# Kernel optimization log

Measured on AMD Instinct MI355X. Metric: run time of the kernel, lower is better.

Reference implementation:

```python
import jax, jax.numpy as jnp
import numpy as np

N_NODES = 100000
N_EDGES = 3200000
IN_DIM = 11
HID = 32


def setup_inputs() -> dict:
    key = jax.random.key(0)
    ks = jax.random.split(key, 12)
    inp = {
        "x": jax.random.normal(ks[0], (N_NODES, IN_DIM), dtype=jnp.float32),
        "edge_index": jax.random.randint(ks[1], (2, N_EDGES), 0, N_NODES, dtype=jnp.int32),
        "batch": jnp.zeros((N_NODES,), dtype=jnp.int32),
        # GCNConv layer 1 (11 -> 32)
        "W1": jax.random.normal(ks[2], (IN_DIM, HID), dtype=jnp.float32) / np.sqrt(IN_DIM),
        "b1": jnp.zeros((HID,), dtype=jnp.float32),
        # GCNConv layer 2 (32 -> 32)
        "W2": jax.random.normal(ks[3], (HID, HID), dtype=jnp.float32) / np.sqrt(HID),
        "b2": jnp.zeros((HID,), dtype=jnp.float32),
        # output MLP: 32 -> 16 -> 1
        "Wo1": jax.random.normal(ks[4], (HID, HID // 2), dtype=jnp.float32) / np.sqrt(HID),
        "bo1": jnp.zeros((HID // 2,), dtype=jnp.float32),
        "Wo2": jax.random.normal(ks[5], (HID // 2, 1), dtype=jnp.float32) / np.sqrt(HID // 2),
        "bo2": jnp.zeros((1,), dtype=jnp.float32),
    }
    return inp


def _gcn_norm(edge_index, n_nodes):
    # Add self-loops and compute symmetric normalization (PyG GCNConv default).
    loops = jnp.arange(n_nodes, dtype=edge_index.dtype)
    src = jnp.concatenate([edge_index[0], loops])
    dst = jnp.concatenate([edge_index[1], loops])
    ones = jnp.ones_like(dst, dtype=jnp.float32)
    deg = jax.ops.segment_sum(ones, dst, num_segments=n_nodes)  # degree of A+I on target side
    dinv = jax.lax.rsqrt(deg)  # deg >= 1 thanks to self-loops
    norm = dinv[src] * dinv[dst]  # [E+N]
    return src, dst, norm


def _gcn_conv(x, W, b, src, dst, norm, n_nodes):
    xw = x @ W                                   # transform first (small dim)
    msg = norm[:, None] * xw[src]                # gather + scale  [E+N, H]
    agg = jax.ops.segment_sum(msg, dst, num_segments=n_nodes)  # scatter-add
    return agg + b


def reference(x, edge_index, batch, W1, b1, W2, b2, Wo1, bo1, Wo2, bo2):
    n = x.shape[0]
    src, dst, norm = _gcn_norm(edge_index, n)
    h = jax.nn.relu(_gcn_conv(x, W1, b1, src, dst, norm, n))
    # F.dropout(training=self.training) is identity in eval mode
    h = jax.nn.relu(_gcn_conv(h, W2, b2, src, dst, norm, n))
    h = jax.nn.elu(h @ Wo1 + bo1)
    out = h @ Wo2 + bo2
    return out.squeeze(-1)  # [N]
```

## Files before the change

kernel.cpp:

```cpp
#include <hip/hip_runtime.h>
#include <hip/hip_fp16.h>
#include <math.h>

#define N_NODES 100000
#define N_EDGES 3200000
#define IN_DIM 11
#define HID 32
#define HID2 16
#define SCHUNK 100352
#define BINSHIFT 8
#define BINSZ 256
#define NB 391
#define CHUNK 6144
#define NCH 521
#define NCH1 522
#define FCAP 9216

__device__ __forceinline__ int wincl(int v) {
    int lane = threadIdx.x & 63;
#pragma unroll
    for (int d = 1; d < 64; d <<= 1) {
        int u = __shfl_up(v, d, 64);
        v += (lane >= d) ? u : 0;
    }
    return v;
}

__device__ __forceinline__ int blkexcl512(int v, int* wtot) {
    int t = threadIdx.x, lane = t & 63, w = t >> 6;
    int inc = wincl(v);
    if (lane == 63) wtot[w] = inc;
    __syncthreads();
    if (t < 8) {
        int x = wtot[t], ix = x;
#pragma unroll
        for (int d = 1; d < 8; d <<= 1) {
            int u = __shfl_up(ix, d, 64);
            ix += (lane >= d) ? u : 0;
        }
        wtot[t] = ix - x;
    }
    __syncthreads();
    return inc - v + wtot[w];
}

__global__ __launch_bounds__(256) void k_hist(const int* __restrict__ ei,
                                              int* __restrict__ cnthist) {
    __shared__ int h[NB];
    int t = threadIdx.x;
    for (int i = t; i < NB; i += 256) h[i] = 0;
    __syncthreads();
    int b0 = blockIdx.x * CHUNK;
    int n = N_EDGES - b0; if (n > CHUNK) n = CHUNK;
    for (int e = t * 4; e < n; e += 1024) {
        int4 d4 = *(const int4*)(ei + N_EDGES + b0 + e);
        atomicAdd(&h[d4.x >> BINSHIFT], 1);
        atomicAdd(&h[d4.y >> BINSHIFT], 1);
        atomicAdd(&h[d4.z >> BINSHIFT], 1);
        atomicAdd(&h[d4.w >> BINSHIFT], 1);
    }
    __syncthreads();
    for (int i = t; i < NB; i += 256)
        cnthist[i * NCH1 + blockIdx.x] = h[i];
}

__global__ __launch_bounds__(256) void k_colscan(int* __restrict__ cnthist,
                                                 int* __restrict__ colsum) {
    __shared__ int wtot[4];
    int i = blockIdx.x;
    int t = threadIdx.x;
    int lane = t & 63;
    int v[4];
    int s4 = 0;
#pragma unroll
    for (int u = 0; u < 4; ++u) {
        int idx = t * 4 + u;
        v[u] = (idx < NCH) ? cnthist[i * NCH1 + idx] : 0;
        s4 += v[u];
    }
    int inc = wincl(s4);
    if (lane == 63) wtot[t >> 6] = inc;
    __syncthreads();
    if (t < 4) {
        int x = wtot[t], ix = x;
#pragma unroll
        for (int d = 1; d < 4; d <<= 1) {
            int u2 = __shfl_up(ix, d, 64);
            ix += (lane >= d) ? u2 : 0;
        }
        wtot[t] = ix - x;
    }
    __syncthreads();
    int base = inc - s4 + wtot[t >> 6];
#pragma unroll
    for (int u = 0; u < 4; ++u) {
        int idx = t * 4 + u;
        if (idx < NCH) cnthist[i * NCH1 + idx] = base;
        base += v[u];
    }
    if (t == 255) {
        cnthist[i * NCH1 + NCH] = base;
        colsum[i] = base;
    }
}

__global__ __launch_bounds__(512) void k_scanbins(const int* __restrict__ colsum,
                                                  int* __restrict__ binbase) {
    __shared__ int wtot[8];
    int t = threadIdx.x;
    int v = (t < NB) ? colsum[t] : 0;
    int pre = blkexcl512(v, wtot);
    if (t < NB) binbase[t] = pre;
    if (t == 0) binbase[NB] = N_EDGES;
}

__global__ __launch_bounds__(512) void k_binscatter(const int* __restrict__ ei,
                                                    const int* __restrict__ binbase,
                                                    const int* __restrict__ cnthist,
                                                    unsigned* __restrict__ binbuf) {
    __shared__ unsigned       srecS[CHUNK];
    __shared__ unsigned short sbinS[CHUNK];
    __shared__ int h[NB], rl[NB], gb[NB];
    __shared__ int wtot[8];
    int t = threadIdx.x;
    int b0 = blockIdx.x * CHUNK;
    int n = N_EDGES - b0; if (n > CHUNK) n = CHUNK;
    int pre_b = 0, c = 0;
    if (t < NB) {
        pre_b = cnthist[t * NCH1 + blockIdx.x];
        c = cnthist[t * NCH1 + blockIdx.x + 1] - pre_b;
    }
    int rlv = blkexcl512(c, wtot);
    if (t < NB) {
        rl[t] = rlv;
        gb[t] = binbase[t] + pre_b;
        h[t] = 0;
    }
    __syncthreads();
    for (int e = t; e < n; e += 512) {
        int d = ei[N_EDGES + b0 + e];
        int s = ei[b0 + e];
        int b = d >> BINSHIFT;
        int p = rl[b] + atomicAdd(&h[b], 1);
        srecS[p] = (unsigned)s | ((unsigned)(d & (BINSZ - 1)) << 17);
        sbinS[p] = (unsigned short)b;
    }
    __syncthreads();
    for (int p = t; p < n; p += 512) {
        int b = sbinS[p];
        binbuf[gb[b] + (p - rl[b])] = srecS[p];
    }
}

__global__ __launch_bounds__(512) void k_binfill(const unsigned* __restrict__ binbuf,
                                                 const int* __restrict__ binbase,
                                                 int* __restrict__ rowstart,
                                                 float* __restrict__ dinv,
                                                 int* __restrict__ csr_src) {
    int bb = blockIdx.x;
    int b = bb >> 1;
    int half = bb & 1;
    int t = threadIdx.x;
    __shared__ unsigned srec[FCAP];
    __shared__ int cnt[BINSZ], rloc[BINSZ], cur[BINSZ], wtot[8];
    int ebeg = binbase[b], eend = binbase[b + 1];
    int m = eend - ebeg;
    if (t < BINSZ) cnt[t] = 0;
    __syncthreads();
    for (int e = t; e < m; e += 512) {
        unsigned v = binbuf[ebeg + e];
        if (e < FCAP) srec[e] = v;
        atomicAdd(&cnt[v >> 17], 1);
    }
    __syncthreads();
    int c = (t < BINSZ) ? cnt[t] : 0;
    int pre = blkexcl512(c, wtot);
    if (t < BINSZ) {
        rloc[t] = pre;
        cur[t] = 0;
        int node = b * BINSZ + t;
        if ((t >> 7) == half && node < N_NODES) {
            rowstart[node] = ebeg + pre;
            dinv[node] = rsqrtf((float)c + 1.0f);
        }
    }
    if (bb == 0 && t == 0) rowstart[N_NODES] = N_EDGES;
    __syncthreads();
    for (int e = t; e < m; e += 512) {
        unsigned vv = (e < FCAP) ? srec[e] : binbuf[ebeg + e];
        int dl = vv >> 17;
        if ((dl >> 7) == half) {
            int p = ebeg + rloc[dl] + atomicAdd(&cur[dl], 1);
            csr_src[p] = (int)(vv & 0x1FFFFu);
        }
    }
}

__global__ void k_xw1(const float* __restrict__ x, const float* __restrict__ W1,
                      const float* __restrict__ dinv, __half* __restrict__ xwh) {
    int t = blockIdx.x * blockDim.x + threadIdx.x;
    int node = t >> 5;
    int j = t & 31;
    __shared__ float sW[IN_DIM * HID];
    __shared__ float sx[8 * IN_DIM];
    for (int i = threadIdx.x; i < IN_DIM * HID; i += 256) sW[i] = W1[i];
    int base = blockIdx.x * 8;
    if (threadIdx.x < 8 * IN_DIM) sx[threadIdx.x] = x[base * IN_DIM + threadIdx.x];
    __syncthreads();
    int ln = node - base;
    float acc = 0.0f;
#pragma unroll
    for (int k = 0; k < IN_DIM; ++k)
        acc += sx[ln * IN_DIM + k] * sW[k * HID + j];
    xwh[t] = __float2half(dinv[node] * acc);
}

__device__ __forceinline__ void accum8(float* __restrict__ acc, const uint4 v) {
    float2 f0 = __half22float2(*(const __half2*)&v.x);
    float2 f1 = __half22float2(*(const __half2*)&v.y);
    float2 f2 = __half22float2(*(const __half2*)&v.z);
    float2 f3 = __half22float2(*(const __half2*)&v.w);
    acc[0] += f0.x; acc[1] += f0.y;
    acc[2] += f1.x; acc[3] += f1.y;
    acc[4] += f2.x; acc[5] += f2.y;
    acc[6] += f3.x; acc[7] += f3.y;
}

__device__ __forceinline__ void edge_accum8(int beg, int end, int q, int oj,
                                            const int* __restrict__ csr_src,
                                            const __half* __restrict__ xwh,
                                            float* __restrict__ acc) {
#pragma unroll
    for (int k = 0; k < 8; ++k) acc[k] = 0.0f;
    int e = beg;
    for (; e + 32 <= end; e += 32) {
        int s0 = csr_src[e + q];
        int s1 = csr_src[e + 8 + q];
        int s2 = csr_src[e + 16 + q];
        int s3 = csr_src[e + 24 + q];
        uint4 v0 = *(const uint4*)(xwh + ((s0 << 5) | oj));
        uint4 v1 = *(const uint4*)(xwh + ((s1 << 5) | oj));
        uint4 v2 = *(const uint4*)(xwh + ((s2 << 5) | oj));
        uint4 v3 = *(const uint4*)(xwh + ((s3 << 5) | oj));
        accum8(acc, v0); accum8(acc, v1); accum8(acc, v2); accum8(acc, v3);
    }
    if (e + 16 <= end) {
        int s0 = csr_src[e + q];
        int s1 = csr_src[e + 8 + q];
        uint4 v0 = *(const uint4*)(xwh + ((s0 << 5) | oj));
        uint4 v1 = *(const uint4*)(xwh + ((s1 << 5) | oj));
        accum8(acc, v0); accum8(acc, v1);
        e += 16;
    }
    if (e + 8 <= end) {
        int s0 = csr_src[e + q];
        uint4 v0 = *(const uint4*)(xwh + ((s0 << 5) | oj));
        accum8(acc, v0);
        e += 8;
    }
    if (e + q < end) {
        int s0 = csr_src[e + q];
        uint4 v0 = *(const uint4*)(xwh + ((s0 << 5) | oj));
        accum8(acc, v0);
    }
#pragma unroll
    for (int m = 4; m <= 16; m <<= 1) {
#pragma unroll
        for (int k = 0; k < 8; ++k) acc[k] += __shfl_xor(acc[k], m);
    }
}

__global__ __launch_bounds__(256) void k_gather_xw2(const int* __restrict__ rowstart,
                                                    const float* __restrict__ dinv,
                                                    const int* __restrict__ csr_src,
                                                    const __half* __restrict__ xwh1,
                                                    const float* __restrict__ b1,
                                                    const float* __restrict__ W2,
                                                    __half* __restrict__ xwh2) {
    __shared__ float sW2[HID * HID];
    __shared__ float sA[8][33];
    __shared__ float sH[8][33];
    for (int i = threadIdx.x; i < HID * HID; i += 256) sW2[i] = W2[i];

    int ln = threadIdx.x >> 5;
    int node = blockIdx.x * 8 + ln;
    int l = threadIdx.x & 31;
    int q = l >> 2;
    int oj = (l & 3) << 3;

    float acc[8];
    edge_accum8(rowstart[node], rowstart[node + 1], q, oj, csr_src, xwh1, acc);
    if (q == 0) {
#pragma unroll
        for (int k = 0; k < 8; ++k) sA[ln][oj + k] = acc[k];
    }
    __syncthreads();

    int j = l;
    float dd = dinv[node];
    float hv = dd * (sA[ln][j] + __half2float(xwh1[node * HID + j])) + b1[j];
    sH[ln][j] = hv > 0.0f ? hv : 0.0f;
    __syncthreads();

    float a2 = 0.0f;
#pragma unroll
    for (int k = 0; k < HID; ++k) a2 += sH[ln][k] * sW2[k * HID + j];
    xwh2[node * HID + j] = __float2half(dd * a2);
}

__global__ __launch_bounds__(256) void k_gather_mlp(const int* __restrict__ rowstart,
                                                    const float* __restrict__ dinv,
                                                    const int* __restrict__ csr_src,
                                                    const __half* __restrict__ xwh,
                                                    const float* __restrict__ b2,
                                                    const float* __restrict__ Wo1,
                                                    const float* __restrict__ bo1,
                                                    const float* __restrict__ Wo2,
                                                    const float* __restrict__ bo2,
                                                    float* __restrict__ out) {
    __shared__ float sW1[HID * HID2];
    __shared__ float sb1[HID2];
    __shared__ float sW2v[HID2];
    __shared__ float sb2[HID];
    __shared__ float sA[8][33];
    __shared__ float sH[8][33];
    for (int i = threadIdx.x; i < HID * HID2; i += 256) sW1[i] = Wo1[i];
    if (threadIdx.x < HID2) {
        sb1[threadIdx.x] = bo1[threadIdx.x];
        sW2v[threadIdx.x] = Wo2[threadIdx.x];
    }
    if (threadIdx.x < HID) sb2[threadIdx.x] = b2[threadIdx.x];

    int ln = threadIdx.x >> 5;
    int node = blockIdx.x * 8 + ln;
    int l = threadIdx.x & 31;
    int q = l >> 2;
    int oj = (l & 3) << 3;

    float acc[8];
    edge_accum8(rowstart[node], rowstart[node + 1], q, oj, csr_src, xwh, acc);
    if (q == 0) {
#pragma unroll
        for (int k = 0; k < 8; ++k) sA[ln][oj + k] = acc[k];
    }
    __syncthreads();

    int j = l;
    float dd = dinv[node];
    float hv = dd * (sA[ln][j] + __half2float(xwh[node * HID + j])) + sb2[j];
    sH[ln][j] = hv > 0.0f ? hv : 0.0f;
    __syncthreads();

    float val = 0.0f;
    if (j < HID2) {
        float a = sb1[j];
#pragma unroll
        for (int k = 0; k < HID; ++k) a += sH[ln][k] * sW1[k * HID2 + j];
        a = a > 0.0f ? a : (expf(a) - 1.0f);
        val = a * sW2v[j];
    }
#pragma unroll
    for (int d = 16; d >= 1; d >>= 1) val += __shfl_down(val, d, 32);
    if (j == 0) out[node] = val + bo2[0];
}

extern "C" void kernel_launch(void* const* d_in, const int* in_sizes, int n_in,
                              void* d_out, int out_size, void* d_ws, size_t ws_size,
                              hipStream_t stream) {
    const float* x   = (const float*)d_in[0];
    const int*   ei  = (const int*)d_in[1];
    const float* W1  = (const float*)d_in[3];
    const float* b1  = (const float*)d_in[4];
    const float* W2  = (const float*)d_in[5];
    const float* b2  = (const float*)d_in[6];
    const float* Wo1 = (const float*)d_in[7];
    const float* bo1 = (const float*)d_in[8];
    const float* Wo2 = (const float*)d_in[9];
    const float* bo2 = (const float*)d_in[10];
    float* out = (float*)d_out;

    int*      colsum   = (int*)d_ws;
    int*      binbase  = colsum + 512;
    int*      rowstart = binbase + 512;
    float*    dinv     = (float*)(rowstart + SCHUNK);
    int*      csr_src  = (int*)(dinv + SCHUNK);
    unsigned* binbuf   = (unsigned*)(csr_src + N_EDGES);
    __half*   XWH1     = (__half*)(binbuf + N_EDGES);
    __half*   XWH2     = XWH1 + (size_t)N_NODES * HID;
    int*      cnthist  = csr_src;

    const int BT = 256;
    int gNH  = (N_NODES * HID + BT - 1) / BT;
    int gG   = N_NODES / 8;

    k_hist      <<<NCH, BT, 0, stream>>>(ei, cnthist);
    k_colscan   <<<NB, BT, 0, stream>>>(cnthist, colsum);
    k_scanbins  <<<1, 512, 0, stream>>>(colsum, binbase);
    k_binscatter<<<NCH, 512, 0, stream>>>(ei, binbase, cnthist, binbuf);
    k_binfill   <<<2 * NB, 512, 0, stream>>>(binbuf, binbase, rowstart, dinv, csr_src);

    k_xw1<<<gNH, BT, 0, stream>>>(x, W1, dinv, XWH1);
    k_gather_xw2<<<gG, BT, 0, stream>>>(rowstart, dinv, csr_src, XWH1, b1, W2, XWH2);

    k_gather_mlp<<<gG, BT, 0, stream>>>(rowstart, dinv, csr_src, XWH2,
                                        b2, Wo1, bo1, Wo2, bo2, out);
}
```

Before: 239.4 us.

## Split CSR rows by source half and gather in two phased passes per block

The CSR build now sorts each destination row's edges by whether the source node falls in the lower or upper half of the node range. The split point is packed into the upper bits of rowstart. Each gather block now handles 64 nodes: it first accumulates all lower-half-source edges for those nodes, then all upper-half-source edges. The aim is to shrink the working set of feature rows being gathered at any moment and so improve cache hit rates. In exchange it adds extra syncs, a serial loop of 8 node groups per block, fewer blocks, and a packing scheme that limits edge offsets to 22 bits and counts to 10 bits.

```diff
diff --git a/kernel.cpp b/kernel.cpp
--- a/kernel.cpp
+++ b/kernel.cpp
@@ -15,6 +15,9 @@
 #define NCH 521
 #define NCH1 522
 #define FCAP 9216
+#define NHALF 50000
+#define GN 64
+#define GB 1563
 
 __device__ __forceinline__ int wincl(int v) {
     int lane = threadIdx.x & 63;
@@ -162,36 +165,43 @@
     int half = bb & 1;
     int t = threadIdx.x;
     __shared__ unsigned srec[FCAP];
-    __shared__ int cnt[BINSZ], rloc[BINSZ], cur[BINSZ], wtot[8];
+    __shared__ int cnt[512], rloc[512], cur[512], wtot[8];
     int ebeg = binbase[b], eend = binbase[b + 1];
     int m = eend - ebeg;
-    if (t < BINSZ) cnt[t] = 0;
+    cnt[t] = 0;
     __syncthreads();
     for (int e = t; e < m; e += 512) {
         unsigned v = binbuf[ebeg + e];
         if (e < FCAP) srec[e] = v;
-        atomicAdd(&cnt[v >> 17], 1);
-    }
-    __syncthreads();
-    int c = (t < BINSZ) ? cnt[t] : 0;
+        int s = (int)(v & 0x1FFFFu);
+        int key = (int)((v >> 17) << 1) | (s >= NHALF);
+        atomicAdd(&cnt[key], 1);
+    }
+    __syncthreads();
+    int c = cnt[t];
     int pre = blkexcl512(c, wtot);
-    if (t < BINSZ) {
-        rloc[t] = pre;
-        cur[t] = 0;
-        int node = b * BINSZ + t;
-        if ((t >> 7) == half && node < N_NODES) {
-            rowstart[node] = ebeg + pre;
-            dinv[node] = rsqrtf((float)c + 1.0f);
+    rloc[t] = pre;
+    cur[t] = 0;
+    if ((t & 1) == 0) {
+        int mloc = t >> 1;
+        int node = b * BINSZ + mloc;
+        if ((mloc >> 7) == half && node < N_NODES) {
+            int tot = c + cnt[t + 1];
+            unsigned u = (unsigned)(ebeg + pre) | ((unsigned)c << 22);
+            rowstart[node] = (int)u;
+            dinv[node] = rsqrtf((float)tot + 1.0f);
         }
     }
     if (bb == 0 && t == 0) rowstart[N_NODES] = N_EDGES;
     __syncthreads();
     for (int e = t; e < m; e += 512) {
         unsigned vv = (e < FCAP) ? srec[e] : binbuf[ebeg + e];
-        int dl = vv >> 17;
+        int dl = (int)(vv >> 17);
         if ((dl >> 7) == half) {
-            int p = ebeg + rloc[dl] + atomicAdd(&cur[dl], 1);
-            csr_src[p] = (int)(vv & 0x1FFFFu);
+            int s = (int)(vv & 0x1FFFFu);
+            int key = (dl << 1) | (s >= NHALF);
+            int p = ebeg + rloc[key] + atomicAdd(&cur[key], 1);
+            csr_src[p] = s;
         }
     }
 }
@@ -226,12 +236,10 @@
     acc[6] += f3.x; acc[7] += f3.y;
 }
 
-__device__ __forceinline__ void edge_accum8(int beg, int end, int q, int oj,
+__device__ __forceinline__ void edge_range8(int beg, int end, int q, int oj,
                                             const int* __restrict__ csr_src,
                                             const __half* __restrict__ xwh,
                                             float* __restrict__ acc) {
-#pragma unroll
-    for (int k = 0; k < 8; ++k) acc[k] = 0.0f;
     int e = beg;
     for (; e + 32 <= end; e += 32) {
         int s0 = csr_src[e + q];
@@ -263,10 +271,13 @@
         uint4 v0 = *(const uint4*)(xwh + ((s0 << 5) | oj));
         accum8(acc, v0);
     }
-#pragma unroll
-    for (int m = 4; m <= 16; m <<= 1) {
-#pragma unroll
-        for (int k = 0; k < 8; ++k) acc[k] += __shfl_xor(acc[k], m);
+}
+
+__device__ __forceinline__ void octet_reduce(float* __restrict__ acc) {
+#pragma unroll
+    for (int m2 = 4; m2 <= 16; m2 <<= 1) {
+#pragma unroll
+        for (int k = 0; k < 8; ++k) acc[k] += __shfl_xor(acc[k], m2);
     }
 }
 
@@ -278,34 +289,66 @@
                                                     const float* __restrict__ W2,
                                                     __half* __restrict__ xwh2) {
     __shared__ float sW2[HID * HID];
-    __shared__ float sA[8][33];
+    __shared__ float stash[8][8][33];
     __shared__ float sH[8][33];
     for (int i = threadIdx.x; i < HID * HID; i += 256) sW2[i] = W2[i];
 
     int ln = threadIdx.x >> 5;
-    int node = blockIdx.x * 8 + ln;
     int l = threadIdx.x & 31;
     int q = l >> 2;
     int oj = (l & 3) << 3;
-
-    float acc[8];
-    edge_accum8(rowstart[node], rowstart[node + 1], q, oj, csr_src, xwh1, acc);
-    if (q == 0) {
-#pragma unroll
-        for (int k = 0; k < 8; ++k) sA[ln][oj + k] = acc[k];
-    }
-    __syncthreads();
-
-    int j = l;
-    float dd = dinv[node];
-    float hv = dd * (sA[ln][j] + __half2float(xwh1[node * HID + j])) + b1[j];
-    sH[ln][j] = hv > 0.0f ? hv : 0.0f;
-    __syncthreads();
-
-    float a2 = 0.0f;
-#pragma unroll
-    for (int k = 0; k < HID; ++k) a2 += sH[ln][k] * sW2[k * HID + j];
-    xwh2[node * HID + j] = __float2half(dd * a2);
+    int base = blockIdx.x * GN;
+
+#pragma unroll 1
+    for (int i = 0; i < 8; ++i) {
+        int node = base + i * 8 + ln;
+        unsigned v0 = (node < N_NODES) ? (unsigned)rowstart[node] : 0u;
+        int rs = (int)(v0 & 0x3FFFFFu);
+        int mid = rs + (int)(v0 >> 22);
+        float acc[8];
+#pragma unroll
+        for (int k = 0; k < 8; ++k) acc[k] = 0.0f;
+        edge_range8(rs, mid, q, oj, csr_src, xwh1, acc);
+        octet_reduce(acc);
+        if (q == 0) {
+#pragma unroll
+            for (int k = 0; k < 8; ++k) stash[i][ln][oj + k] = acc[k];
+        }
+    }
+    __syncthreads();
+#pragma unroll 1
+    for (int i = 0; i < 8; ++i) {
+        int node = base + i * 8 + ln;
+        int ok = node < N_NODES;
+        unsigned v0 = ok ? (unsigned)rowstart[node] : 0u;
+        unsigned v1 = ok ? (unsigned)rowstart[node + 1] : 0u;
+        int rs = (int)(v0 & 0x3FFFFFu);
+        int mid = rs + (int)(v0 >> 22);
+        int re = (int)(v1 & 0x3FFFFFu);
+        float acc[8];
+#pragma unroll
+        for (int k = 0; k < 8; ++k) acc[k] = 0.0f;
+        edge_range8(mid, re, q, oj, csr_src, xwh1, acc);
+        octet_reduce(acc);
+        if (q == 0) {
+#pragma unroll
+            for (int k = 0; k < 8; ++k) stash[i][ln][oj + k] += acc[k];
+        }
+        __syncthreads();
+        float dd = ok ? dinv[node] : 0.0f;
+        if (ok) {
+            float hv = dd * (stash[i][ln][l] + __half2float(xwh1[node * HID + l])) + b1[l];
+            sH[ln][l] = hv > 0.0f ? hv : 0.0f;
+        }
+        __syncthreads();
+        if (ok) {
+            float a2 = 0.0f;
+#pragma unroll
+            for (int k = 0; k < HID; ++k) a2 += sH[ln][k] * sW2[k * HID + l];
+            xwh2[node * HID + l] = __float2half(dd * a2);
+        }
+        __syncthreads();
+    }
 }
 
 __global__ __launch_bounds__(256) void k_gather_mlp(const int* __restrict__ rowstart,
@@ -322,7 +365,7 @@
     __shared__ float sb1[HID2];
     __shared__ float sW2v[HID2];
     __shared__ float sb2[HID];
-    __shared__ float sA[8][33];
+    __shared__ float stash[8][8][33];
     __shared__ float sH[8][33];
     for (int i = threadIdx.x; i < HID * HID2; i += 256) sW1[i] = Wo1[i];
     if (threadIdx.x < HID2) {
@@ -332,36 +375,66 @@
     if (threadIdx.x < HID) sb2[threadIdx.x] = b2[threadIdx.x];
 
     int ln = threadIdx.x >> 5;
-    int node = blockIdx.x * 8 + ln;
     int l = threadIdx.x & 31;
     int q = l >> 2;
     int oj = (l & 3) << 3;
-
-    float acc[8];
-    edge_accum8(rowstart[node], rowstart[node + 1], q, oj, csr_src, xwh, acc);
-    if (q == 0) {
-#pragma unroll
-        for (int k = 0; k < 8; ++k) sA[ln][oj + k] = acc[k];
-    }
-    __syncthreads();
-
-    int j = l;
-    float dd = dinv[node];
-    float hv = dd * (sA[ln][j] + __half2float(xwh[node * HID + j])) + sb2[j];
-    sH[ln][j] = hv > 0.0f ? hv : 0.0f;
-    __syncthreads();
-
-    float val = 0.0f;
-    if (j < HID2) {
-        float a = sb1[j];
-#pragma unroll
-        for (int k = 0; k < HID; ++k) a += sH[ln][k] * sW1[k * HID2 + j];
-        a = a > 0.0f ? a : (expf(a) - 1.0f);
-        val = a * sW2v[j];
-    }
-#pragma unroll
-    for (int d = 16; d >= 1; d >>= 1) val += __shfl_down(val, d, 32);
-    if (j == 0) out[node] = val + bo2[0];
+    int base = blockIdx.x * GN;
+
+#pragma unroll 1
+    for (int i = 0; i < 8; ++i) {
+        int node = base + i * 8 + ln;
+        unsigned v0 = (node < N_NODES) ? (unsigned)rowstart[node] : 0u;
+        int rs = (int)(v0 & 0x3FFFFFu);
+        int mid = rs + (int)(v0 >> 22);
+        float acc[8];
+#pragma unroll
+        for (int k = 0; k < 8; ++k) acc[k] = 0.0f;
+        edge_range8(rs, mid, q, oj, csr_src, xwh, acc);
+        octet_reduce(acc);
+        if (q == 0) {
+#pragma unroll
+            for (int k = 0; k < 8; ++k) stash[i][ln][oj + k] = acc[k];
+        }
+    }
+    __syncthreads();
+#pragma unroll 1
+    for (int i = 0; i < 8; ++i) {
+        int node = base + i * 8 + ln;
+        int ok = node < N_NODES;
+        unsigned v0 = ok ? (unsigned)rowstart[node] : 0u;
+        unsigned v1 = ok ? (unsigned)rowstart[node + 1] : 0u;
+        int rs = (int)(v0 & 0x3FFFFFu);
+        int mid = rs + (int)(v0 >> 22);
+        int re = (int)(v1 & 0x3FFFFFu);
+        float acc[8];
+#pragma unroll
+        for (int k = 0; k < 8; ++k) acc[k] = 0.0f;
+        edge_range8(mid, re, q, oj, csr_src, xwh, acc);
+        octet_reduce(acc);
+        if (q == 0) {
+#pragma unroll
+            for (int k = 0; k < 8; ++k) stash[i][ln][oj + k] += acc[k];
+        }
+        __syncthreads();
+        if (ok) {
+            float dd = dinv[node];
+            float hv = dd * (stash[i][ln][l] + __half2float(xwh[node * HID + l])) + sb2[l];
+            sH[ln][l] = hv > 0.0f ? hv : 0.0f;
+        }
+        __syncthreads();
+        float val = 0.0f;
+        if (ok && l < HID2) {
+            float a = sb1[l];
+#pragma unroll
+            for (int k = 0; k < HID; ++k) a += sH[ln][k] * sW1[k * HID2 + l];
+            a = a > 0.0f ? a : (expf(a) - 1.0f);
+            val = a * sW2v[l];
+        }
+#pragma unroll
+        for (int d = 16; d >= 1; d >>= 1) val += __shfl_down(val, d, 32);
+        if (ok && l == 0) out[node] = val + bo2[0];
+        __syncthreads();
+    }
 }
 
 extern "C" void kernel_launch(void* const* d_in, const int* in_sizes, int n_in,
@@ -391,7 +464,6 @@
 
     const int BT = 256;
     int gNH  = (N_NODES * HID + BT - 1) / BT;
-    int gG   = N_NODES / 8;
 
     k_hist      <<<NCH, BT, 0, stream>>>(ei, cnthist);
     k_colscan   <<<NB, BT, 0, stream>>>(cnthist, colsum);
@@ -400,8 +472,8 @@
     k_binfill   <<<2 * NB, 512, 0, stream>>>(binbuf, binbase, rowstart, dinv, csr_src);
 
     k_xw1<<<gNH, BT, 0, stream>>>(x, W1, dinv, XWH1);
-    k_gather_xw2<<<gG, BT, 0, stream>>>(rowstart, dinv, csr_src, XWH1, b1, W2, XWH2);
-
-    k_gather_mlp<<<gG, BT, 0, stream>>>(rowstart, dinv, csr_src, XWH2,
+    k_gather_xw2<<<GB, BT, 0, stream>>>(rowstart, dinv, csr_src, XWH1, b1, W2, XWH2);
+
+    k_gather_mlp<<<GB, BT, 0, stream>>>(rowstart, dinv, csr_src, XWH2,
                                         b2, Wo1, bo1, Wo2, bo2, out);
 }
```

New measurement: 280.0 us. +17.0%, slower.
